# Kernel tuning notes

Hardware: AMD Instinct MI355X
Metric: run time of the kernel (lower is better)

## Reference

```python
import jax, jax.numpy as jnp
import numpy as np
from jax.scipy.special import logsumexp

K, D, H, A = 8, 512, 512, 1024
S, T = 64, 128
B = S * T


def setup_inputs() -> dict:
    key = jax.random.key(0)
    k1, k2, k3, k4 = jax.random.split(key, 4)
    obs = jax.random.normal(k1, (B, D), dtype=jnp.float32)
    actions = jax.random.randint(k2, (B,), 0, A, dtype=jnp.int64)
    # uniform mixture prior (log(1/K)) => all components supported
    start_mixture_logprobs = jnp.full((S, K), jnp.log(1.0 / K), dtype=jnp.float32)
    W1 = jax.random.normal(k3, (K, D, H), dtype=jnp.float32) * 0.02
    b1 = jnp.zeros((K, H), dtype=jnp.float32)
    W2 = jax.random.normal(k4, (K, H, A), dtype=jnp.float32) * 0.02
    b2 = jnp.zeros((K, A), dtype=jnp.float32)
    return {"obs": obs, "actions": actions,
            "start_mixture_logprobs": start_mixture_logprobs,
            "W1": W1, "b1": b1, "W2": W2, "b2": b2, "seq_len": T}


def reference(obs, actions, start_mixture_logprobs, W1, b1, W2, b2, seq_len):
    num_seqs, num_comp = start_mixture_logprobs.shape
    batch = obs.shape[0]
    t_len = batch // num_seqs  # == seq_len
    num_out = W2.shape[-1]

    # per-component MLP on the full batch (all components supported)
    h = jax.nn.relu(jnp.einsum('bd,kdh->kbh', obs, W1) + b1[:, None, :])
    logits = jnp.einsum('kbh,kha->kba', h, W2) + b2[:, None, :]  # [K,B,A]
    component_logprobs = jax.nn.log_softmax(logits, axis=2)      # [K,B,A]

    # add time dimension: [B, K, A] -> [S, T, K, A]
    clp_t = component_logprobs.transpose(1, 0, 2).reshape(num_seqs, t_len, num_comp, num_out)
    act_t = actions.reshape(num_seqs, t_len)

    # gather logprob of taken action per component: [S, T, K]
    idx = jnp.broadcast_to(act_t[:, :, None, None], (num_seqs, t_len, num_comp, 1))
    action_logprobs = jnp.take_along_axis(clp_t, idx, axis=3)[..., 0]
    cum = jnp.cumsum(action_logprobs, axis=1)  # [S,T,K]

    # per-timestep posterior over mixture (shifted cumulative evidence)
    shift = jnp.concatenate([jnp.zeros((num_seqs, 1, num_comp), dtype=cum.dtype), cum[:, :-1]], axis=1)
    mix = jax.nn.log_softmax(start_mixture_logprobs[:, None, :] + shift, axis=2)  # [S,T,K]
    final_mixture_logprobs = jax.nn.log_softmax(start_mixture_logprobs + cum[:, -1], axis=1)

    # combine: logsumexp over components of component_logprobs + mixture logprob
    mix_flat = mix.reshape(batch, num_comp).T  # [K,B]
    model_out = logsumexp(component_logprobs + mix_flat[:, :, None], axis=0)  # [B,A]
    return model_out, final_mixture_logprobs
```

## Files before the change

### kernel.cpp

```cpp
#include <hip/hip_runtime.h>
#include <hip/hip_bf16.h>
#include <stdint.h>

#define KC   8
#define DIM  512
#define HID  512
#define ACTN 1024
#define NS   64
#define NT   128
#define NB   8192
#define PB   8

typedef __attribute__((ext_vector_type(8))) short short8;
typedef __attribute__((ext_vector_type(8))) unsigned short ushort8;
typedef __attribute__((ext_vector_type(4))) float floatx4;
typedef __attribute__((ext_vector_type(2))) float floatx2;
typedef __attribute__((ext_vector_type(4))) unsigned int uint4v;

__device__ inline float bf2f(unsigned short u) {
    return __uint_as_float(((unsigned int)u) << 16);
}
__device__ inline unsigned short f2bf_rne(float x) {
    unsigned int u = __float_as_uint(x);
    u += 0x7fffu + ((u >> 16) & 1u);
    return (unsigned short)(u >> 16);
}

__device__ inline int csw(int row, int col) {
    return (row << 7) + (col ^ ((row & 7) << 3));
}

__device__ inline unsigned char f2fp8_manual(float v) {
    unsigned int s = (__float_as_uint(v) >> 24) & 0x80u;
    float a = fabsf(v) * 0x1.0p-120f;
    unsigned int b = __float_as_uint(a);
    b += 0x7FFFFu + ((b >> 20) & 1u);
    unsigned int m = b >> 20;
    if (m > 0x7Eu) m = 0x7Eu;
    return (unsigned char)(s | m);
}
__device__ inline float fp82f_manual(unsigned int byte) {
    unsigned int bits = ((byte & 0x80u) << 24) | ((byte & 0x7Fu) << 20);
    return __uint_as_float(bits) * 0x1.0p+120f;
}
template <bool HI>
__device__ inline unsigned int pk_fp8(float a, float b, unsigned int old) {
#if __has_builtin(__builtin_amdgcn_cvt_pk_fp8_f32)
    return __builtin_amdgcn_cvt_pk_fp8_f32(a, b, old, HI);
#else
    unsigned int p = (unsigned int)f2fp8_manual(a) | ((unsigned int)f2fp8_manual(b) << 8);
    return HI ? ((old & 0x0000ffffu) | (p << 16)) : ((old & 0xffff0000u) | p);
#endif
}
template <bool HI>
__device__ inline floatx2 unpk_fp8(unsigned int src) {
#if __has_builtin(__builtin_amdgcn_cvt_pk_f32_fp8)
    return __builtin_amdgcn_cvt_pk_f32_fp8(src, HI);
#else
    unsigned int w = HI ? (src >> 16) : src;
    floatx2 r;
    r.x = fp82f_manual(w & 0xffu);
    r.y = fp82f_manual((w >> 8) & 0xffu);
    return r;
#endif
}

__device__ inline void gload_lds16(const unsigned short* g, unsigned short* l) {
    __builtin_amdgcn_global_load_lds(
        (const __attribute__((address_space(1))) unsigned int*)g,
        (__attribute__((address_space(3))) unsigned int*)l,
        16, 0, 0);
}

__global__ __launch_bounds__(256) void prep_kernel(
    const float* __restrict__ obs, const float* __restrict__ W1,
    const float* __restrict__ W2,
    unsigned short* __restrict__ obs_bk, unsigned short* __restrict__ W1bk,
    unsigned short* __restrict__ W2bk)
{
    __shared__ float tile[64][65];
    int id = blockIdx.x;
    if (id < 128) {
        int mg = id;
        const int tx = threadIdx.x & 63, ty = threadIdx.x >> 6;
#pragma unroll
        for (int cc = 0; cc < 8; ++cc) {
            __syncthreads();
#pragma unroll
            for (int i = 0; i < 64; i += 4)
                tile[i + ty][tx] = obs[(size_t)(mg * 64 + i + ty) * DIM + cc * 64 + tx];
            __syncthreads();
#pragma unroll
            for (int rep = 0; rep < 2; ++rep) {
                int idx = rep * 256 + threadIdx.x;
                int c   = idx >> 6;
                int row = idx & 63;
                ushort8 u;
#pragma unroll
                for (int e = 0; e < 8; e++) u[e] = f2bf_rne(tile[row][c * 8 + e]);
                *(ushort8*)(obs_bk + (((size_t)mg * (DIM / 8) + cc * 8 + c) << 9)
                                   + (row << 3)) = u;
            }
        }
        return;
    }
    const float* src; unsigned short* dst; int R, C, xt, yt;
    if (id < 640) {
        int t = id - 128; int z = t >> 6; int rem = t & 63;
        xt = rem & 7; yt = rem >> 3;
        R = DIM; C = HID;
        src = W1 + (size_t)z * DIM * HID; dst = W1bk + (size_t)z * DIM * HID;
    } else {
        int t = id - 640; int z = t >> 7; int rem = t & 127;
        xt = rem & 15; yt = rem >> 4;
        R = HID; C = ACTN;
        src = W2 + (size_t)z * HID * ACTN; dst = W2bk + (size_t)z * HID * ACTN;
    }
    int h0 = xt * 64, d0 = yt * 64;
    int tx = threadIdx.x & 63, ty = threadIdx.x >> 6;
#pragma unroll
    for (int i = 0; i < 64; i += 4)
        tile[ty + i][tx] = src[(size_t)(d0 + ty + i) * C + h0 + tx];
    __syncthreads();
    int KCHR = R >> 3;
#pragma unroll
    for (int rep = 0; rep < 2; ++rep) {
        int idx  = rep * 256 + threadIdx.x;
        int h_l  = idx & 63;
        int dc_l = idx >> 6;
        ushort8 u;
#pragma unroll
        for (int e = 0; e < 8; e++) u[e] = f2bf_rne(tile[dc_l * 8 + e][h_l]);
        size_t off = ((((size_t)(h0 >> 6) * KCHR) + (d0 >> 3) + dc_l) << 9) + (h_l << 3);
        *(ushort8*)(dst + off) = u;
    }
}

__global__ __launch_bounds__(256, 4) void gemm_blk_kernel(
    const unsigned short* __restrict__ Aall,
    const unsigned short* __restrict__ Ball,
    const float* __restrict__ biasall,
    void* __restrict__ Call,
    const int* __restrict__ actions,
    float* __restrict__ psum, float* __restrict__ palp,
    int M, int N, int Kd,
    long long zsA, long long zsB,
    int strideBias, long long strideCbytes,
    int do_relu, int do_lse, int do_blocked)
{
    __shared__ __align__(16) unsigned short S[16384];
    unsigned short* const As = S;
    unsigned short* const Bs = S + 8192;

    const int zb = blockIdx.z;
    const float* bias = biasall + (size_t)zb * strideBias;
    char* const Cbase = (char*)Call + (size_t)zb * strideCbytes;

    const int tid  = threadIdx.x;
    const int lane = tid & 63;
    const int wave = tid >> 6;
    const int wm = wave >> 1;
    const int wn = wave & 1;
    const int quad = lane >> 4;
    const int l16  = lane & 15;

    const int bm = blockIdx.x * 128;
    const int bn = blockIdx.y * 128;
    const int KCH = Kd >> 3;

    floatx4 acc[4][4];
#pragma unroll
    for (int i = 0; i < 4; i++)
#pragma unroll
        for (int j = 0; j < 4; j++)
            acc[i][j] = (floatx4){0.f, 0.f, 0.f, 0.f};

    const int loff = lane << 3;
    const unsigned short* pA = Aall + (size_t)zb * zsA + (((size_t)(bm >> 6) * KCH + wave) << 9) + loff;
    const unsigned short* pB = Ball + (size_t)zb * zsB + (((size_t)(bn >> 6) * KCH + wave) << 9) + loff;
    const size_t mgs = (size_t)KCH << 9;
    unsigned short* ldsA = As + wave * 1024;
    unsigned short* ldsB = Bs + wave * 1024;

    const int nk = Kd >> 6;
    for (int it = 0; it < nk; ++it) {
        __syncthreads();
        gload_lds16(pA,              ldsA);
        gload_lds16(pA + mgs,        ldsA + 512);
        gload_lds16(pA + 2048,       ldsA + 4096);
        gload_lds16(pA + 2048 + mgs, ldsA + 4096 + 512);
        gload_lds16(pB,              ldsB);
        gload_lds16(pB + mgs,        ldsB + 512);
        gload_lds16(pB + 2048,       ldsB + 4096);
        gload_lds16(pB + 2048 + mgs, ldsB + 4096 + 512);
        pA += 4096; pB += 4096;
        __syncthreads();

#pragma unroll
        for (int h = 0; h < 2; ++h) {
            const unsigned short* Ah = As + h * 4096 + quad * 1024;
            const unsigned short* Bh = Bs + h * 4096 + quad * 1024;
            short8 af[4], bfr[4];
#pragma unroll
            for (int i = 0; i < 4; i++)
                af[i] = *(const short8*)(Ah + ((wm * 64 + i * 16 + l16) << 3));
#pragma unroll
            for (int j = 0; j < 4; j++)
                bfr[j] = *(const short8*)(Bh + ((wn * 64 + j * 16 + l16) << 3));
#pragma unroll
            for (int i = 0; i < 4; i++)
#pragma unroll
                for (int j = 0; j < 4; j++)
                    acc[i][j] = __builtin_amdgcn_mfma_f32_16x16x32_bf16(
                        af[i], bfr[j], acc[i][j], 0, 0, 0);
        }
    }
    __syncthreads();

    unsigned short* const Cs = S;
#pragma unroll
    for (int j = 0; j < 4; j++) {
        int col = wn * 64 + j * 16 + l16;
        float bv = bias[bn + col];
#pragma unroll
        for (int i = 0; i < 4; i++) {
            int rw = wm * 64 + i * 16 + quad * 4;
#pragma unroll
            for (int r = 0; r < 4; r++) {
                float v = acc[i][j][r] + bv;
                if (do_relu) v = fmaxf(v, 0.f);
                Cs[csw(rw + r, col)] = f2bf_rne(v);
            }
        }
    }
    __syncthreads();

    if (do_blocked) {
        unsigned short* Cb16 = (unsigned short*)Cbase;
        const int KCHo = N >> 3;
#pragma unroll
        for (int rep = 0; rep < 8; ++rep) {
            int idx  = rep * 256 + tid;
            int kc_l = idx >> 7;
            int row  = idx & 127;
            ushort8 u = *(const ushort8*)&Cs[csw(row, kc_l << 3)];
            size_t off = ((((size_t)((bm >> 6) + (row >> 6)) * KCHo) + (bn >> 3) + kc_l) << 9)
                       + ((row & 63) << 3);
            *(ushort8*)(Cb16 + off) = u;
        }
    } else {
        unsigned char* Cb8 = (unsigned char*)Cbase;
        const int row = tid >> 1;
        const int ch  = (tid & 1) * 64;
        unsigned char* crow = Cb8 + (size_t)(bm + row) * N + bn + ch;

        float s = 0.f;
#pragma unroll
        for (int g = 0; g < 4; g++) {
            ushort8 u0 = *(const ushort8*)&Cs[csw(row, ch + 16 * g)];
            ushort8 u1 = *(const ushort8*)&Cs[csw(row, ch + 16 * g + 8)];
            float v[16];
#pragma unroll
            for (int e = 0; e < 8; e++) { v[e] = bf2f(u0[e]); v[8 + e] = bf2f(u1[e]); }
#pragma unroll
            for (int e = 0; e < 16; e++) s += __expf(v[e]);
            uint4v pk;
            pk.x = pk_fp8<true>(v[2],  v[3],  pk_fp8<false>(v[0],  v[1],  0u));
            pk.y = pk_fp8<true>(v[6],  v[7],  pk_fp8<false>(v[4],  v[5],  0u));
            pk.z = pk_fp8<true>(v[10], v[11], pk_fp8<false>(v[8],  v[9],  0u));
            pk.w = pk_fp8<true>(v[14], v[15], pk_fp8<false>(v[12], v[13], 0u));
            *(uint4v*)(crow + 16 * g) = pk;
        }

        float stot = s + __shfl_xor(s, 1);
        size_t kb = (size_t)zb * M + bm + row;
        if ((tid & 1) == 0)
            psum[kb * PB + blockIdx.y] = stot;
        int act = actions[bm + row];
        int rel = act - bn;
        if (rel >= ch && rel < ch + 64)
            palp[kb] = bf2f(Cs[csw(row, rel)]);
    }
}

__global__ __launch_bounds__(128) void mix_kernel(
    const float* __restrict__ palp,
    const float* __restrict__ psum,
    const float* __restrict__ start,
    float* __restrict__ w,
    float* __restrict__ fmix)
{
    __shared__ float buf[2][NT][9];
    int s = blockIdx.x, t = threadIdx.x;
    int b = s * NT + t;

    float a[KC], lsev[KC];
#pragma unroll
    for (int k = 0; k < KC; k++) {
        size_t kb = (size_t)k * NB + b;
        const floatx4* pv = (const floatx4*)(psum + kb * PB);
        floatx4 s0 = pv[0], s1 = pv[1];
        float Ssum = (s0.x + s0.y + s0.z + s0.w) + (s1.x + s1.y + s1.z + s1.w);
        float l = __logf(Ssum);
        lsev[k] = l;
        a[k] = palp[kb] - l;
    }

#pragma unroll
    for (int k = 0; k < KC; k++) buf[0][t][k] = a[k];
    int p = 0;
    for (int off = 1; off < NT; off <<= 1) {
        __syncthreads();
#pragma unroll
        for (int k = 0; k < KC; k++) {
            float x = buf[p][t][k];
            if (t >= off) x += buf[p][t - off][k];
            buf[1 - p][t][k] = x;
        }
        p ^= 1;
    }
    __syncthreads();
    float st[KC], e[KC];
#pragma unroll
    for (int k = 0; k < KC; k++) st[k] = start[s * KC + k];
#pragma unroll
    for (int k = 0; k < KC; k++) e[k] = st[k] + buf[p][t][k] - a[k];
    float m = e[0];
#pragma unroll
    for (int k = 1; k < KC; k++) m = fmaxf(m, e[k]);
    float sum = 0.f;
#pragma unroll
    for (int k = 0; k < KC; k++) sum += __expf(e[k] - m);
    float l = m + __logf(sum);
#pragma unroll
    for (int k = 0; k < KC; k++)
        w[(size_t)k * NB + b] = (e[k] - l) - lsev[k];

    if (t == NT - 1) {
        float f[KC];
#pragma unroll
        for (int k = 0; k < KC; k++) f[k] = st[k] + buf[p][t][k];
        float m2 = f[0];
#pragma unroll
        for (int k = 1; k < KC; k++) m2 = fmaxf(m2, f[k]);
        float s2 = 0.f;
#pragma unroll
        for (int k = 0; k < KC; k++) s2 += __expf(f[k] - m2);
        float l2 = m2 + __logf(s2);
#pragma unroll
        for (int k = 0; k < KC; k++) fmix[s * KC + k] = f[k] - l2;
    }
}

__global__ __launch_bounds__(256) void combine_kernel(
    const unsigned char* __restrict__ logits8,
    const float* __restrict__ w,
    float* __restrict__ out)
{
    int b  = blockIdx.x * 2 + (threadIdx.x >> 7);
    int a0 = (threadIdx.x & 127) * 8;
    float x[KC][8];
#pragma unroll
    for (int k = 0; k < KC; k++) {
        float wv = w[(size_t)k * NB + b];
        uint2 q = *(const uint2*)(logits8 + ((size_t)k * NB + b) * ACTN + a0);
        floatx2 p01 = unpk_fp8<false>(q.x), p23 = unpk_fp8<true>(q.x);
        floatx2 p45 = unpk_fp8<false>(q.y), p67 = unpk_fp8<true>(q.y);
        x[k][0] = p01.x + wv; x[k][1] = p01.y + wv;
        x[k][2] = p23.x + wv; x[k][3] = p23.y + wv;
        x[k][4] = p45.x + wv; x[k][5] = p45.y + wv;
        x[k][6] = p67.x + wv; x[k][7] = p67.y + wv;
    }
    float* op = out + (size_t)b * ACTN + a0;
#pragma unroll
    for (int j = 0; j < 8; j++) {
        float s = 0.f;
#pragma unroll
        for (int k = 0; k < KC; k++) s += __expf(x[k][j]);
        op[j] = __logf(s);
    }
}

extern "C" void kernel_launch(void* const* d_in, const int* in_sizes, int n_in,
                              void* d_out, int out_size, void* d_ws, size_t ws_size,
                              hipStream_t stream)
{
    const float* obs     = (const float*)d_in[0];
    const int*   actions = (const int*)d_in[1];
    const float* start   = (const float*)d_in[2];
    const float* W1      = (const float*)d_in[3];
    const float* b1      = (const float*)d_in[4];
    const float* W2      = (const float*)d_in[5];
    const float* b2      = (const float*)d_in[6];

    char* ws = (char*)d_ws;
    unsigned short* obs_bk  = (unsigned short*)ws; ws += (size_t)NB * DIM * 2;
    unsigned short* W1bk    = (unsigned short*)ws; ws += (size_t)KC * HID * DIM * 2;
    unsigned short* W2bk    = (unsigned short*)ws; ws += (size_t)KC * ACTN * HID * 2;
    unsigned short* hbuf    = (unsigned short*)ws; ws += (size_t)KC * NB * HID * 2;
    unsigned char*  logits8 = (unsigned char*)ws;  ws += (size_t)KC * NB * ACTN;
    float* wbuf = (float*)ws; ws += (size_t)KC * NB * 4;
    float* psum = (float*)ws; ws += (size_t)KC * NB * PB * 4;
    float* palp = (float*)ws; ws += (size_t)KC * NB * 4;

    float* out  = (float*)d_out;
    float* fmix = out + (size_t)NB * ACTN;

    prep_kernel<<<1664, 256, 0, stream>>>(obs, W1, W2, obs_bk, W1bk, W2bk);

    gemm_blk_kernel<<<dim3(NB / 128, HID / 128, KC), 256, 0, stream>>>(
        obs_bk, W1bk, b1, hbuf, actions, psum, palp,
        NB, HID, DIM,
        0LL, (long long)HID * DIM,
        HID, (long long)NB * HID * 2, 1, 0, 1);

    gemm_blk_kernel<<<dim3(NB / 128, ACTN / 128, KC), 256, 0, stream>>>(
        hbuf, W2bk, b2, logits8, actions, psum, palp,
        NB, ACTN, HID,
        (long long)NB * HID, (long long)ACTN * HID,
        ACTN, (long long)NB * ACTN, 0, 1, 0);

    mix_kernel<<<NS, NT, 0, stream>>>(palp, psum, start, wbuf, fmix);

    combine_kernel<<<NB / 2, 256, 0, stream>>>(logits8, wbuf, out);
}
```

Measured before the change: 246.4 us.

## Double-buffer GEMM K-loop in LDS and transpose psum layout for coalescing

The GEMM main loop now processes 32-wide K chunks and uses two LDS buffers, issuing the global-to-LDS loads for the next chunk before computing on the current one. This drops one of the two barriers per iteration and is meant to hide global load latency behind the MFMA work. Separately, the partial softmax sums are stored as [PB][K][M] instead of [K*M][PB], so the epilogue stores and the mix kernel reads become coalesced across threads. The trade-off is twice as many loop iterations, each doing less MFMA work per barrier.

```diff
diff --git a/kernel.cpp b/kernel.cpp
--- a/kernel.cpp
+++ b/kernel.cpp
@@ -149,8 +149,6 @@
     int do_relu, int do_lse, int do_blocked)
 {
     __shared__ __align__(16) unsigned short S[16384];
-    unsigned short* const As = S;
-    unsigned short* const Bs = S + 8192;
 
     const int zb = blockIdx.z;
     const float* bias = biasall + (size_t)zb * strideBias;
@@ -176,46 +174,45 @@
             acc[i][j] = (floatx4){0.f, 0.f, 0.f, 0.f};
 
     const int loff = lane << 3;
-    const unsigned short* pA = Aall + (size_t)zb * zsA + (((size_t)(bm >> 6) * KCH + wave) << 9) + loff;
-    const unsigned short* pB = Ball + (size_t)zb * zsB + (((size_t)(bn >> 6) * KCH + wave) << 9) + loff;
+    const unsigned short* baseA = Aall + (size_t)zb * zsA + (((size_t)(bm >> 6) * KCH + wave) << 9) + loff;
+    const unsigned short* baseB = Ball + (size_t)zb * zsB + (((size_t)(bn >> 6) * KCH + wave) << 9) + loff;
     const size_t mgs = (size_t)KCH << 9;
-    unsigned short* ldsA = As + wave * 1024;
-    unsigned short* ldsB = Bs + wave * 1024;
-
-    const int nk = Kd >> 6;
+
+    auto stage = [&](int c, int kc) {
+        unsigned short* SA = S + c * 8192 + wave * 1024;
+        unsigned short* SB = SA + 4096;
+        const unsigned short* gA = baseA + ((size_t)kc << 9);
+        const unsigned short* gB = baseB + ((size_t)kc << 9);
+        gload_lds16(gA,       SA);
+        gload_lds16(gA + mgs, SA + 512);
+        gload_lds16(gB,       SB);
+        gload_lds16(gB + mgs, SB + 512);
+    };
+
+    const int nk = Kd >> 5;
+    stage(0, 0);
+    __syncthreads();
+    int c = 0;
     for (int it = 0; it < nk; ++it) {
+        if (it + 1 < nk) stage(c ^ 1, (it + 1) * 4);
+        const unsigned short* Ah = S + c * 8192 + quad * 1024;
+        const unsigned short* Bh = Ah + 4096;
+        short8 af[4], bfr[4];
+#pragma unroll
+        for (int i = 0; i < 4; i++)
+            af[i] = *(const short8*)(Ah + ((wm * 64 + i * 16 + l16) << 3));
+#pragma unroll
+        for (int j = 0; j < 4; j++)
+            bfr[j] = *(const short8*)(Bh + ((wn * 64 + j * 16 + l16) << 3));
+#pragma unroll
+        for (int i = 0; i < 4; i++)
+#pragma unroll
+            for (int j = 0; j < 4; j++)
+                acc[i][j] = __builtin_amdgcn_mfma_f32_16x16x32_bf16(
+                    af[i], bfr[j], acc[i][j], 0, 0, 0);
         __syncthreads();
-        gload_lds16(pA,              ldsA);
-        gload_lds16(pA + mgs,        ldsA + 512);
-        gload_lds16(pA + 2048,       ldsA + 4096);
-        gload_lds16(pA + 2048 + mgs, ldsA + 4096 + 512);
-        gload_lds16(pB,              ldsB);
-        gload_lds16(pB + mgs,        ldsB + 512);
-        gload_lds16(pB + 2048,       ldsB + 4096);
-        gload_lds16(pB + 2048 + mgs, ldsB + 4096 + 512);
-        pA += 4096; pB += 4096;
-        __syncthreads();
-
-#pragma unroll
-        for (int h = 0; h < 2; ++h) {
-            const unsigned short* Ah = As + h * 4096 + quad * 1024;
-            const unsigned short* Bh = Bs + h * 4096 + quad * 1024;
-            short8 af[4], bfr[4];
-#pragma unroll
-            for (int i = 0; i < 4; i++)
-                af[i] = *(const short8*)(Ah + ((wm * 64 + i * 16 + l16) << 3));
-#pragma unroll
-            for (int j = 0; j < 4; j++)
-                bfr[j] = *(const short8*)(Bh + ((wn * 64 + j * 16 + l16) << 3));
-#pragma unroll
-            for (int i = 0; i < 4; i++)
-#pragma unroll
-                for (int j = 0; j < 4; j++)
-                    acc[i][j] = __builtin_amdgcn_mfma_f32_16x16x32_bf16(
-                        af[i], bfr[j], acc[i][j], 0, 0, 0);
-        }
-    }
-    __syncthreads();
+        c ^= 1;
+    }
 
     unsigned short* const Cs = S;
 #pragma unroll
@@ -275,7 +272,7 @@
         float stot = s + __shfl_xor(s, 1);
         size_t kb = (size_t)zb * M + bm + row;
         if ((tid & 1) == 0)
-            psum[kb * PB + blockIdx.y] = stot;
+            psum[((size_t)blockIdx.y * KC + zb) * M + bm + row] = stot;
         int act = actions[bm + row];
         int rel = act - bn;
         if (rel >= ch && rel < ch + 64)
@@ -298,9 +295,10 @@
 #pragma unroll
     for (int k = 0; k < KC; k++) {
         size_t kb = (size_t)k * NB + b;
-        const floatx4* pv = (const floatx4*)(psum + kb * PB);
-        floatx4 s0 = pv[0], s1 = pv[1];
-        float Ssum = (s0.x + s0.y + s0.z + s0.w) + (s1.x + s1.y + s1.z + s1.w);
+        float Ssum = 0.f;
+#pragma unroll
+        for (int p2 = 0; p2 < PB; p2++)
+            Ssum += psum[((size_t)p2 * KC + k) * NB + b];
         float l = __logf(Ssum);
         lsev[k] = l;
         a[k] = palp[kb] - l;
```

Result: no change. 251.1 us (+1.9%).
